# Optimization experiments

Measured on AMD Instinct MI355X. Metric: run time of the kernel, lower is better.

## Reference

```python
import math
import jax, jax.numpy as jnp
import numpy as np

B, N, D = 8, 2048, 256
NUM_ROLES = 3
ROLE_HUB, ROLE_MONITOR = 1, 2  # assumed ROLE_TO_ID mapping
NEG = -10000.0


def _lin_init(k, fan_in, shape):
    b = 1.0 / math.sqrt(fan_in)
    return jax.random.uniform(k, shape, jnp.float32, -b, b)


def setup_inputs() -> dict:
    key = jax.random.key(0)
    ks = jax.random.split(key, 20)
    inp = {
        'x': jax.random.normal(ks[0], (B, N, D), jnp.float32),
        'node_roles': jax.random.randint(ks[1], (B, N), 0, NUM_ROLES),
        'node_mask': jax.random.bernoulli(ks[2], 0.9, (B, N)),
        'ln_gamma': jnp.ones((D,), jnp.float32),
        'ln_beta': jnp.zeros((D,), jnp.float32),
        'role_emb': jax.random.normal(ks[3], (NUM_ROLES, D), jnp.float32),
    }
    names = ['q', 'k', 's', 'p', 'o']
    for i, nm in enumerate(names):
        inp['W' + nm] = _lin_init(ks[4 + 2 * i], D, (D, D))
        inp['b' + nm] = _lin_init(ks[5 + 2 * i], D, (D,))
    inp['Wg'] = _lin_init(ks[14], 2 * D, (2 * D, D))
    inp['bg'] = _lin_init(ks[15], 2 * D, (D,))
    return inp


def _layernorm(x, g, b):
    mu = jnp.mean(x, -1, keepdims=True)
    var = jnp.mean(jnp.square(x - mu), -1, keepdims=True)
    return (x - mu) * jax.lax.rsqrt(var + 1e-5) * g + b


def reference(x, node_roles, node_mask, ln_gamma, ln_beta, role_emb,
              Wq, bq, Wk, bk, Ws, bs, Wp, bp, Wo, bo, Wg, bg):
    normed = _layernorm(x, ln_gamma, ln_beta)
    role_bias = role_emb[node_roles]                      # [B,N,D]
    h = normed + role_bias
    query = h @ Wq + bq
    key_t = h @ Wk + bk
    sender = h @ Ws + bs
    payload = normed @ Wp + bp

    read_logits = jnp.einsum('bid,bjd->bij', query, key_t) / math.sqrt(D)
    fs = role_bias + sender
    forward_logits = jnp.einsum('bid,bjd->bij', fs, fs)
    logits = read_logits + 0.5 * forward_logits           # variant='selective'

    source_mask = node_mask                               # variant != 'memory_hubs'
    pair_mask = node_mask[:, :, None] & source_mask[:, None, :]
    eye = jnp.eye(N, dtype=bool)[None]
    pair_mask = pair_mask | (eye & node_mask[:, :, None] & node_mask[:, None, :])

    logits = jnp.where(pair_mask, logits, NEG)
    weights = jax.nn.softmax(logits, axis=-1)
    weights = jnp.where(pair_mask, weights, 0.0)

    message = jnp.einsum('bij,bjd->bid', weights, payload)
    gate = jax.nn.sigmoid(jnp.concatenate([x, message], axis=-1) @ Wg + bg)
    update = (gate * message) @ Wo + bo
    out = x + update                                      # dropout p=0

    entropy = -(weights * jnp.log(weights + 1e-8)).sum(-1).mean()
    # masked-mean replicates torch's weights[..., col_mask].mean() without dynamic shapes
    mon_cols = (node_roles == ROLE_MONITOR).any(0)        # [N]
    hub_cols = (node_roles == ROLE_HUB).any(0)
    def col_mean(cols):
        cnt = cols.sum() * B * N
        tot = (weights * cols[None, None, :].astype(weights.dtype)).sum()
        return jnp.where(cnt > 0, tot / jnp.maximum(cnt, 1), 0.0)
    return (out, entropy, col_mean(mon_cols), col_mean(hub_cols))
```

## Files before the change

### kernel.cpp

```cpp
#include <hip/hip_runtime.h>
#include <math.h>

#define BB 8
#define NN 2048
#define DD 256
#define MTOK 16384

typedef __bf16 bf16x8 __attribute__((ext_vector_type(8)));
typedef __bf16 bf16x4 __attribute__((ext_vector_type(4)));
typedef float f32x4 __attribute__((ext_vector_type(4)));

#define MFMA16(a, b, c) __builtin_amdgcn_mfma_f32_16x16x32_bf16(a, b, c, 0, 0, 0)

#define BARX()                              \
  do {                                      \
    asm volatile("" ::: "memory");          \
    __builtin_amdgcn_s_barrier();           \
    asm volatile("" ::: "memory");          \
  } while (0)
#define WAITVM(N)                                              \
  do {                                                         \
    asm volatile("s_waitcnt vmcnt(" #N ")" ::: "memory");      \
    __builtin_amdgcn_sched_barrier(0);                         \
  } while (0)

#define OFF_X16    0ull
#define OFF_N16    2097152ull
#define OFF_H16    4194304ull
#define OFF_GROW   8388608ull
#define OFF_GCOL   12582912ull
#define OFF_PTE    16777216ull
#define OFF_WT     19005440ull
#define OFF_STAT   19234816ull
#define OFF_ENT    23625728ull
#define OFF_MONR   23642112ull
#define OFF_HUBR   23658496ull
#define OFF_MONF   23674880ull
#define OFF_HUBF   23676928ull
#define OFF_MASK   23678976ull
#define OFF_PART   23683072ull
#define OFF_MSGN0  OFF_N16
#define OFF_MSGN1  OFF_H16
#define OFF_MSG16  OFF_PTE
#define OFF_GM16   OFF_GROW

__device__ __forceinline__ void gl_lds16(const void* g, void* l) {
  __builtin_amdgcn_global_load_lds(
      (const __attribute__((address_space(1))) unsigned int*)g,
      (__attribute__((address_space(3))) unsigned int*)l, 16, 0, 0);
}

__global__ __launch_bounds__(256) void setup_kernel(
    const float* __restrict__ x, const int* __restrict__ roles,
    const void* __restrict__ mraw,
    const float* __restrict__ gamma, const float* __restrict__ beta,
    const float* __restrict__ role_emb,
    const float* __restrict__ Wq, const float* __restrict__ Wk,
    const float* __restrict__ Ws, const float* __restrict__ Wp,
    const float* __restrict__ Wg, const float* __restrict__ Wo,
    __bf16* __restrict__ X16, __bf16* __restrict__ N16,
    __bf16* __restrict__ H16, __bf16* __restrict__ WT,
    unsigned char* __restrict__ mask8,
    float* __restrict__ monf, float* __restrict__ hubf) {
  __shared__ float T[64][65];
  int bid = blockIdx.x;
  int tid = threadIdx.x;
  if (bid < 4096) {
    int t = bid * 4 + (tid >> 6);
    int lane = tid & 63;
    size_t off = (size_t)t * DD + lane * 4;
    float4 xv = *(const float4*)(x + off);
    float s = xv.x + xv.y + xv.z + xv.w;
    float ss = xv.x * xv.x + xv.y * xv.y + xv.z * xv.z + xv.w * xv.w;
#pragma unroll
    for (int m = 1; m < 64; m <<= 1) {
      s += __shfl_xor(s, m, 64);
      ss += __shfl_xor(ss, m, 64);
    }
    float mu = s * (1.0f / 256.0f);
    float var = ss * (1.0f / 256.0f) - mu * mu;
    float inv = rsqrtf(var + 1e-5f);
    float4 g = *(const float4*)(gamma + lane * 4);
    float4 be = *(const float4*)(beta + lane * 4);
    float nv[4];
    nv[0] = (xv.x - mu) * inv * g.x + be.x;
    nv[1] = (xv.y - mu) * inv * g.y + be.y;
    nv[2] = (xv.z - mu) * inv * g.z + be.z;
    nv[3] = (xv.w - mu) * inv * g.w + be.w;
    int role = roles[t];
    float4 rb = *(const float4*)(role_emb + (size_t)role * DD + lane * 4);
    float rbv[4] = {rb.x, rb.y, rb.z, rb.w};
    bf16x4 xo, no, ho;
    float xf[4] = {xv.x, xv.y, xv.z, xv.w};
#pragma unroll
    for (int q = 0; q < 4; ++q) {
      xo[q] = (__bf16)xf[q];
      no[q] = (__bf16)nv[q];
      ho[q] = (__bf16)(nv[q] + rbv[q]);
    }
    *(bf16x4*)&X16[off] = xo;
    *(bf16x4*)&N16[off] = no;
    *(bf16x4*)&H16[off] = ho;
  } else if (bid < 4288) {
    int wblk = bid - 4096;
    int z = wblk >> 5, rem = wblk & 31;
    int bx = rem & 3, by = rem >> 2;
    const float* src;
    int K;
    size_t doff;
    switch (z) {
      case 0: src = Wq; K = 256; doff = 0; break;
      case 1: src = Wk; K = 256; doff = 65536; break;
      case 2: src = Ws; K = 256; doff = 131072; break;
      case 3: src = Wp; K = 256; doff = 196608; break;
      case 4: src = Wg; K = 512; doff = 262144; break;
      default: src = Wo; K = 256; doff = 393216; break;
    }
    int k0 = by * 64;
    if (k0 >= K) return;
    int n0 = bx * 64;
#pragma unroll
    for (int p = 0; p < 16; ++p) {
      int idx = p * 256 + tid;
      int r = idx >> 6, c = idx & 63;
      T[r][c] = src[(size_t)(k0 + r) * 256 + n0 + c];
    }
    __syncthreads();
#pragma unroll
    for (int p = 0; p < 16; ++p) {
      int idx = p * 256 + tid;
      int n = idx >> 6, k = idx & 63;
      WT[doff + (size_t)(n0 + n) * K + k0 + k] = (__bf16)T[k][n];
    }
  } else {
    int* csh = (int*)&T[0][0];
    if (tid == 0) { csh[0] = 0; csh[1] = 0; }
    __syncthreads();
    const unsigned char* raw = (const unsigned char*)mraw;
    int c0 = 0, c1 = 0;
    for (int i = tid; i < 4096; i += 256) {
      int nz = (raw[i] != 0) ? 1 : 0;
      if ((i & 3) == 0) c0 += nz; else c1 += nz;
    }
    atomicAdd(&csh[0], c0);
    atomicAdd(&csh[1], c1);
    __syncthreads();
    int k = (csh[0] == 0) ? 2 : ((csh[1] == 0) ? 0 : 1);
    int t = (bid - 4288) * 256 + tid;
    if (t < MTOK) {
      int v;
      if (k == 1)      v = (raw[t] != 0);
      else if (k == 0) v = (((const int*)mraw)[t] != 0);
      else             v = (((const float*)mraw)[t] != 0.0f);
      mask8[t] = (unsigned char)v;
    }
    if (t < NN) {
      int mon = 0, hub = 0;
#pragma unroll
      for (int b = 0; b < BB; ++b) {
        int r = roles[b * NN + t];
        mon |= (r == 2) ? 1 : 0;
        hub |= (r == 1) ? 1 : 0;
      }
      monf[t] = (float)mon;
      hubf[t] = (float)hub;
    }
  }
}

__global__ __launch_bounds__(256) void fill_pte_kernel(
    const int* __restrict__ roles, __bf16* __restrict__ PTE) {
  int idx = blockIdx.x * 256 + threadIdx.x;
  int b = idx >> 11, col = idx & 2047;
  int mon = 0, hub = 0;
#pragma unroll
  for (int bb = 0; bb < BB; ++bb) {
    int r = roles[bb * NN + col];
    mon |= (r == 2) ? 1 : 0;
    hub |= (r == 1) ? 1 : 0;
  }
  size_t rbase = ((size_t)(b * 272 + 256)) * 2048 + col;
  PTE[rbase] = (__bf16)(float)mon;
  PTE[rbase + 2048] = (__bf16)(float)hub;
  PTE[rbase + 2 * 2048] = (__bf16)1.0f;
#pragma unroll
  for (int r = 3; r < 16; ++r) PTE[rbase + (size_t)r * 2048] = (__bf16)0.0f;
}

__global__ __launch_bounds__(256, 3) void proj4_kernel(
    const __bf16* __restrict__ H16, const __bf16* __restrict__ N16,
    const __bf16* __restrict__ WT,
    const float* __restrict__ bq, const float* __restrict__ bk,
    const float* __restrict__ bs, const float* __restrict__ bp,
    const int* __restrict__ roles, const float* __restrict__ remb,
    __bf16* __restrict__ Grow, __bf16* __restrict__ Gcol,
    __bf16* __restrict__ PTE) {
  __shared__ __align__(16) unsigned char As[128 * 128];
  __shared__ __align__(16) unsigned char Bs[128 * 128];
  int z = blockIdx.z;
  const __bf16* A = (z == 3) ? N16 : H16;
  const __bf16* W = WT + (size_t)z * 65536;
  const float* bias = (z == 0) ? bq : (z == 1) ? bk : (z == 2) ? bs : bp;

  int tid = threadIdx.x;
  int w = tid >> 6, lane = tid & 63, ln15 = lane & 15, lq = lane >> 4;
  int wr = w >> 1, wc = w & 1;
  int row0 = blockIdx.y * 128, col0 = blockIdx.x * 128;
  f32x4 acc[4][4];
#pragma unroll
  for (int i = 0; i < 4; ++i)
#pragma unroll
    for (int j = 0; j < 4; ++j) acc[i][j] = (f32x4){0.f, 0.f, 0.f, 0.f};

  int lr = lane >> 3;
  int sb = ((lane & 7) * 16) ^ ((lr & 7) << 4);

  for (int kt = 0; kt < 4; ++kt) {
    __syncthreads();
#pragma unroll
    for (int i2 = 0; i2 < 4; ++i2) {
      int idx = w * 4 + i2;
      int grow = row0 + idx * 8 + lr;
      gl_lds16((const unsigned char*)A + (size_t)grow * 512 + kt * 128 + sb,
               As + idx * 1024);
    }
#pragma unroll
    for (int i2 = 0; i2 < 4; ++i2) {
      int idx = w * 4 + i2;
      int gcol = col0 + idx * 8 + lr;
      gl_lds16((const unsigned char*)W + (size_t)gcol * 512 + kt * 128 + sb,
               Bs + idx * 1024);
    }
    __syncthreads();
#pragma unroll
    for (int ks = 0; ks < 2; ++ks) {
      bf16x8 af[4], bfr[4];
#pragma unroll
      for (int i = 0; i < 4; ++i) {
        int rl = wr * 64 + i * 16 + ln15;
        int byteoff = (lq * 16 + ks * 64) ^ ((rl & 7) << 4);
        af[i] = *(const bf16x8*)(As + rl * 128 + byteoff);
      }
#pragma unroll
      for (int j = 0; j < 4; ++j) {
        int cl = wc * 64 + j * 16 + ln15;
        int byteoff = (lq * 16 + ks * 64) ^ ((cl & 7) << 4);
        bfr[j] = *(const bf16x8*)(Bs + cl * 128 + byteoff);
      }
#pragma unroll
      for (int i = 0; i < 4; ++i)
#pragma unroll
        for (int j = 0; j < 4; ++j) acc[i][j] = MFMA16(af[i], bfr[j], acc[i][j]);
    }
  }
  float bj[4];
#pragma unroll
  for (int j = 0; j < 4; ++j) bj[j] = bias[col0 + wc * 64 + j * 16 + ln15];
#pragma unroll
  for (int i = 0; i < 4; ++i) {
#pragma unroll
    for (int j = 0; j < 4; ++j) {
      int gcol = col0 + wc * 64 + j * 16 + ln15;
      int growb = row0 + wr * 64 + i * 16 + lq * 4;
      float o[4];
#pragma unroll
      for (int ri = 0; ri < 4; ++ri) o[ri] = acc[i][j][ri] + bj[j];
      if (z == 0) {
#pragma unroll
        for (int ri = 0; ri < 4; ++ri)
          Grow[(size_t)(growb + ri) * 512 + gcol] = (__bf16)(o[ri] * 0.0625f);
      } else if (z == 1) {
#pragma unroll
        for (int ri = 0; ri < 4; ++ri)
          Gcol[(size_t)(growb + ri) * 512 + gcol] = (__bf16)o[ri];
      } else if (z == 2) {
#pragma unroll
        for (int ri = 0; ri < 4; ++ri) {
          float oo = o[ri] + remb[(size_t)roles[growb + ri] * 256 + gcol];
          __bf16 v = (__bf16)(oo * 0.70710678118f);
          Grow[(size_t)(growb + ri) * 512 + 256 + gcol] = v;
          Gcol[(size_t)(growb + ri) * 512 + 256 + gcol] = v;
        }
      } else {
        bf16x4 v;
#pragma unroll
        for (int ri = 0; ri < 4; ++ri) v[ri] = (__bf16)o[ri];
        int b = growb >> 11, tok = growb & 2047;
        *(bf16x4*)&PTE[((size_t)(b * 272 + gcol)) * 2048 + tok] = v;
      }
    }
  }
}

__global__ __launch_bounds__(256, 2) void attn_kernel(
    const __bf16* __restrict__ Grow, const __bf16* __restrict__ Gcol,
    const __bf16* __restrict__ PTE, const unsigned char* __restrict__ mask8,
    __bf16* __restrict__ msgn0, __bf16* __restrict__ msgn1,
    float* __restrict__ statP) {
  __shared__ __align__(16) unsigned char GcLo[16384];
  __shared__ __align__(16) unsigned char GcHi[16384];
  __shared__ __align__(16) unsigned char PtS[2][17408];

  int tid = threadIdx.x;
  int w = tid >> 6, lane = tid & 63, ln15 = lane & 15, lq = lane >> 4;
  int id = blockIdx.x;
  int b = id & 7;
  int half = (id >> 3) & 1;
  int r0 = (id >> 4) * 64;
  size_t base = (size_t)b * NN;
  __bf16* msgn = half ? msgn1 : msgn0;
  float* statB = statP + (size_t)half * MTOK * 6;

  const unsigned char* gbase =
      (const unsigned char*)Gcol + (base + half * 1024) * 1024;
  const unsigned char* pbase =
      (const unsigned char*)PTE + (size_t)b * 272 * 4096 + half * 2048;

  bf16x8 Af[16];
  {
    const __bf16* gr = Grow + (base + r0 + w * 16 + ln15) * 512 + lq * 8;
#pragma unroll
    for (int kk = 0; kk < 16; ++kk) Af[kk] = *(const bf16x8*)(gr + kk * 32);
  }

  float m = -1e30f, T = 0.f;
  f32x4 macc[17];
#pragma unroll
  for (int nt = 0; nt < 17; ++nt) macc[nt] = (f32x4){0.f, 0.f, 0.f, 0.f};

  int pswz = (lq ^ ((ln15 >> 1) & 3)) << 4;
  int n0 = ((ln15 >> 2) * 8) + (ln15 & 3);
  int n1 = n0 + 4;
  int s0 = (((n0 & 3) | (((n0 >> 3) & 1) << 2))) << 4;
  int s1 = (((n1 & 3) | (((n1 >> 3) & 1) << 2))) << 4;
  int srcsw = ((lane & 3) ^ ((lane >> 3) & 3)) << 4;
  int glrow = lane >> 5;
  int glb = (lane & 31) * 16;

  auto STG = [&](int ch, unsigned char* dst, int koff) {
#pragma unroll
    for (int i = 0; i < 4; ++i) {
      int rp = w * 8 + 2 * i;
      int r = rp + glrow;
      int sbr = glb ^ ((((r & 3) | (((r >> 3) & 1) << 2))) << 4);
      gl_lds16(gbase + (size_t)(ch * 32 + r) * 1024 + koff + sbr, dst + rp * 512);
    }
  };
  auto STPT = [&](int ch, int buf) {
#pragma unroll
    for (int i = 0; i < 4; ++i) {
      int idx = w * 4 + i;
      int drow = idx * 16 + (lane >> 2);
      gl_lds16(pbase + (size_t)drow * 4096 + ch * 64 + srcsw,
               &PtS[buf][idx * 1024]);
    }
    {
      int drow = 256 + (lane >> 2);
      gl_lds16(pbase + (size_t)drow * 4096 + ch * 64 + srcsw,
               &PtS[buf][16 * 1024]);
    }
  };

  STPT(0, 0);
  STG(0, GcLo, 0);
  STG(0, GcHi, 512);

  for (int ch = 0; ch < 32; ++ch) {
    int cur = ch & 1;
    WAITVM(4);
    BARX();
    STPT(ch + 1, cur ^ 1);

    f32x4 sa0 = (f32x4){0.f, 0.f, 0.f, 0.f};
    f32x4 sa1 = (f32x4){0.f, 0.f, 0.f, 0.f};
    __builtin_amdgcn_s_setprio(1);
#pragma unroll
    for (int kk = 0; kk < 8; ++kk) {
      bf16x8 bv0 = *(const bf16x8*)&GcLo[n0 * 512 + ((lq * 16 + kk * 64) ^ s0)];
      sa0 = MFMA16(bv0, Af[kk], sa0);
      bf16x8 bv1 = *(const bf16x8*)&GcLo[n1 * 512 + ((lq * 16 + kk * 64) ^ s1)];
      sa1 = MFMA16(bv1, Af[kk], sa1);
    }
    __builtin_amdgcn_s_setprio(0);

    WAITVM(5);
    BARX();
    STG(ch + 1, GcLo, 0);

    __builtin_amdgcn_s_setprio(1);
#pragma unroll
    for (int kk = 8; kk < 16; ++kk) {
      bf16x8 bv0 = *(const bf16x8*)&GcHi[n0 * 512 + ((lq * 16 + (kk - 8) * 64) ^ s0)];
      sa0 = MFMA16(bv0, Af[kk], sa0);
      bf16x8 bv1 = *(const bf16x8*)&GcHi[n1 * 512 + ((lq * 16 + (kk - 8) * 64) ^ s1)];
      sa1 = MFMA16(bv1, Af[kk], sa1);
    }
    __builtin_amdgcn_s_setprio(0);

    float sv[8] = {sa0[0], sa0[1], sa0[2], sa0[3], sa1[0], sa1[1], sa1[2], sa1[3]};
    unsigned long long mk = *(const unsigned long long*)(
        mask8 + base + half * 1024 + (size_t)ch * 32 + lq * 8);

    float mt = -1e30f;
#pragma unroll
    for (int i = 0; i < 8; ++i) {
      float li = ((mk >> (8 * i)) & 0xffull) ? sv[i] : -1e30f;
      mt = fmaxf(mt, li);
    }
    mt = fmaxf(mt, __shfl_xor(mt, 16));
    mt = fmaxf(mt, __shfl_xor(mt, 32));
    float mnew = fmaxf(m, mt);
    if (__any(mnew > m + 8.0f)) {
      float ci = __expf(m - mnew);
      float cir[4];
#pragma unroll
      for (int r = 0; r < 4; ++r)
        cir[r] = __shfl(ci, (lane & 48) + ((lane >> 2) & 12) + r);
#pragma unroll
      for (int nt = 0; nt < 17; ++nt) {
        macc[nt][0] *= cir[0]; macc[nt][1] *= cir[1];
        macc[nt][2] *= cir[2]; macc[nt][3] *= cir[3];
      }
      T *= ci;
      m = mnew;
    }
    float e[8], tl = 0.f;
#pragma unroll
    for (int i = 0; i < 8; ++i) {
      float ei = ((mk >> (8 * i)) & 0xffull) ? __expf(sv[i] - m) : 0.f;
      e[i] = ei;
      tl += ei * sv[i];
    }
    tl += __shfl_xor(tl, 16);
    tl += __shfl_xor(tl, 32);
    T += tl;
    bf16x8 ef;
#pragma unroll
    for (int i = 0; i < 8; ++i) ef[i] = (__bf16)e[i];

    __builtin_amdgcn_s_setprio(1);
#pragma unroll
    for (int nt = 0; nt < 17; ++nt) {
      int drow = nt * 16 + ln15;
      bf16x8 pv = *(const bf16x8*)&PtS[cur][drow * 64 + pswz];
      macc[nt] = MFMA16(ef, pv, macc[nt]);
    }
    __builtin_amdgcn_s_setprio(0);

    BARX();
    STG(ch + 1, GcHi, 512);
  }
  WAITVM(0);

#pragma unroll
  for (int r = 0; r < 4; ++r) {
    int grow = r0 + w * 16 + lq * 4 + r;
    size_t row = base + grow;
    float Z = __shfl(macc[16][r], (lane & 48) + 2);
    float invZ = (Z > 0.f) ? (1.0f / Z) : 0.f;
#pragma unroll
    for (int nt = 0; nt < 16; ++nt)
      msgn[row * 256 + nt * 16 + ln15] = (__bf16)(macc[nt][r] * invZ);
    float Tm = __shfl(macc[16][r], (lane & 48) + 0);
    float Th = __shfl(macc[16][r], (lane & 48) + 1);
    float Tr = __shfl(T, (lane & 48) + ((lane >> 2) & 12) + r);
    float mr = __shfl(m, (lane & 48) + ((lane >> 2) & 12) + r);
    if (ln15 == 0) {
      float* stt = statB + row * 6;
      stt[0] = mr; stt[1] = Tr; stt[2] = Z; stt[3] = Tm; stt[4] = Th;
    }
  }
}

__global__ __launch_bounds__(256) void merge_kernel(
    const __bf16* __restrict__ msgn0, const __bf16* __restrict__ msgn1,
    const float* __restrict__ statP, const unsigned char* __restrict__ mask8,
    __bf16* __restrict__ MSG16, float* __restrict__ entr,
    float* __restrict__ monr, float* __restrict__ hubr) {
  int row = blockIdx.x * 4 + (threadIdx.x >> 6);
  int lane = threadIdx.x & 63;
  const float* s0 = statP + (size_t)row * 6;
  const float* s1 = statP + (size_t)(MTOK + row) * 6;
  float m0 = s0[0], T0 = s0[1], Z0 = s0[2], Tm0 = s0[3], Th0 = s0[4];
  float m1 = s1[0], T1 = s1[1], Z1 = s1[2], Tm1 = s1[3], Th1 = s1[4];
  int valid = mask8[row] != 0;
  float mm = fmaxf(m0, m1);
  float c0 = __expf(m0 - mm), c1 = __expf(m1 - mm);
  float w0 = c0 * Z0, w1 = c1 * Z1;
  float Z = w0 + w1;
  int ok = valid && (Z > 0.f);
  float invZ = ok ? (1.0f / Z) : 0.0f;
  float rw0 = w0 * invZ, rw1 = w1 * invZ;
  bf16x4 p0 = *(const bf16x4*)(msgn0 + (size_t)row * 256 + lane * 4);
  bf16x4 p1 = *(const bf16x4*)(msgn1 + (size_t)row * 256 + lane * 4);
  bf16x4 o;
#pragma unroll
  for (int q = 0; q < 4; ++q)
    o[q] = (__bf16)(rw0 * (float)p0[q] + rw1 * (float)p1[q]);
  *(bf16x4*)&MSG16[(size_t)row * 256 + lane * 4] = o;
  if (lane == 0) {
    float T = c0 * T0 + c1 * T1;
    float Tm = c0 * Tm0 + c1 * Tm1;
    float Th = c0 * Th0 + c1 * Th1;
    entr[row] = ok ? (__logf(Z) + mm - T * invZ) : 0.0f;
    monr[row] = ok ? (Tm * invZ) : 0.0f;
    hubr[row] = ok ? (Th * invZ) : 0.0f;
  }
}

template <int K, int MODE>
__global__ __launch_bounds__(256) void gemmb_kernel(
    const __bf16* __restrict__ A0, const __bf16* __restrict__ A1,
    const __bf16* __restrict__ WT, const float* __restrict__ bias,
    const float* __restrict__ xf, const __bf16* __restrict__ msg16,
    void* __restrict__ dst0) {
  __shared__ __align__(16) unsigned char As[128 * 128];
  __shared__ __align__(16) unsigned char Bs[64 * 128];
  int tid = threadIdx.x;
  int w = tid >> 6, lane = tid & 63, ln15 = lane & 15, lq = lane >> 4;
  int wr = w >> 1, wc = w & 1;
  int row0 = blockIdx.y * 128, col0 = blockIdx.x * 64;
  f32x4 acc[4][2];
#pragma unroll
  for (int i = 0; i < 4; ++i)
#pragma unroll
    for (int j = 0; j < 2; ++j) acc[i][j] = (f32x4){0.f, 0.f, 0.f, 0.f};

  int lr = lane >> 3;
  int sb = ((lane & 7) * 16) ^ ((lr & 7) << 4);

  for (int kt = 0; kt < K / 64; ++kt) {
    const __bf16* Ab = A0;
    int ktl = kt;
    if (K == 512 && kt >= 4) { Ab = A1; ktl = kt - 4; }
    __syncthreads();
#pragma unroll
    for (int i2 = 0; i2 < 4; ++i2) {
      int idx = w * 4 + i2;
      int grow = row0 + idx * 8 + lr;
      gl_lds16((const unsigned char*)Ab + (size_t)grow * 512 + ktl * 128 + sb,
               As + idx * 1024);
    }
#pragma unroll
    for (int i2 = 0; i2 < 2; ++i2) {
      int idx = w * 2 + i2;
      int gcol = col0 + idx * 8 + lr;
      gl_lds16((const unsigned char*)WT + (size_t)gcol * (K * 2) + kt * 128 + sb,
               Bs + idx * 1024);
    }
    __syncthreads();
#pragma unroll
    for (int ks = 0; ks < 2; ++ks) {
      bf16x8 af[4], bfr[2];
#pragma unroll
      for (int i = 0; i < 4; ++i) {
        int rl = wr * 64 + i * 16 + ln15;
        int byteoff = (lq * 16 + ks * 64) ^ ((rl & 7) << 4);
        af[i] = *(const bf16x8*)(As + rl * 128 + byteoff);
      }
#pragma unroll
      for (int j = 0; j < 2; ++j) {
        int cl = wc * 32 + j * 16 + ln15;
        int byteoff = (lq * 16 + ks * 64) ^ ((cl & 7) << 4);
        bfr[j] = *(const bf16x8*)(Bs + cl * 128 + byteoff);
      }
#pragma unroll
      for (int i = 0; i < 4; ++i)
#pragma unroll
        for (int j = 0; j < 2; ++j) acc[i][j] = MFMA16(af[i], bfr[j], acc[i][j]);
    }
  }
  float bj[2];
#pragma unroll
  for (int j = 0; j < 2; ++j) bj[j] = bias[col0 + wc * 32 + j * 16 + ln15];
#pragma unroll
  for (int i = 0; i < 4; ++i) {
#pragma unroll
    for (int ri = 0; ri < 4; ++ri) {
      int grow = row0 + wr * 64 + i * 16 + lq * 4 + ri;
#pragma unroll
      for (int j = 0; j < 2; ++j) {
        int gcol = col0 + wc * 32 + j * 16 + ln15;
        float o = acc[i][j][ri] + bj[j];
        if (MODE == 4) {
          float sg = 1.0f / (1.0f + __expf(-o));
          float mv = (float)msg16[(size_t)grow * 256 + gcol];
          ((__bf16*)dst0)[(size_t)grow * 256 + gcol] = (__bf16)(sg * mv);
        } else {
          ((float*)dst0)[(size_t)grow * 256 + gcol] =
              o + xf[(size_t)grow * 256 + gcol];
        }
      }
    }
  }
}

__device__ __forceinline__ float block_sum(float v, float* sh) {
  __syncthreads();
  sh[threadIdx.x] = v;
  __syncthreads();
  for (int s = 128; s > 0; s >>= 1) {
    if ((int)threadIdx.x < s) sh[threadIdx.x] += sh[threadIdx.x + s];
    __syncthreads();
  }
  return sh[0];
}

__global__ __launch_bounds__(256) void reduce1_kernel(
    const float* __restrict__ entr, const float* __restrict__ monr,
    const float* __restrict__ hubr, float* __restrict__ partial) {
  __shared__ float sh[256];
  int t = blockIdx.x * 256 + threadIdx.x;
  float es = entr[t], ms = monr[t], hs = hubr[t];
  float e = block_sum(es, sh);
  float mo = block_sum(ms, sh);
  float hu = block_sum(hs, sh);
  if (threadIdx.x == 0) {
    partial[blockIdx.x * 4 + 0] = e;
    partial[blockIdx.x * 4 + 1] = mo;
    partial[blockIdx.x * 4 + 2] = hu;
  }
}

__global__ __launch_bounds__(256) void reduce2_kernel(
    const float* __restrict__ partial, const float* __restrict__ monf,
    const float* __restrict__ hubf, float* __restrict__ out3) {
  __shared__ float sh[256];
  float es = 0.f, ms = 0.f, hs = 0.f, cmf = 0.f, chf = 0.f;
  if (threadIdx.x < 64) {
    es = partial[threadIdx.x * 4 + 0];
    ms = partial[threadIdx.x * 4 + 1];
    hs = partial[threadIdx.x * 4 + 2];
  }
  for (int j = threadIdx.x; j < NN; j += 256) { cmf += monf[j]; chf += hubf[j]; }
  float esum = block_sum(es, sh);
  float msum = block_sum(ms, sh);
  float hsum = block_sum(hs, sh);
  float cmsum = block_sum(cmf, sh);
  float chsum = block_sum(chf, sh);
  if (threadIdx.x == 0) {
    out3[0] = esum / 16384.0f;
    out3[1] = (cmsum > 0.f) ? (msum / (cmsum * 16384.0f)) : 0.0f;
    out3[2] = (chsum > 0.f) ? (hsum / (chsum * 16384.0f)) : 0.0f;
  }
}

extern "C" void kernel_launch(void* const* d_in, const int* in_sizes, int n_in,
                              void* d_out, int out_size, void* d_ws, size_t ws_size,
                              hipStream_t stream) {
  const float* x = (const float*)d_in[0];
  const int* roles = (const int*)d_in[1];
  const void* mraw = d_in[2];
  const float* gamma = (const float*)d_in[3];
  const float* beta = (const float*)d_in[4];
  const float* remb = (const float*)d_in[5];
  const float* Wq = (const float*)d_in[6];
  const float* bq = (const float*)d_in[7];
  const float* Wk = (const float*)d_in[8];
  const float* bk = (const float*)d_in[9];
  const float* Ws = (const float*)d_in[10];
  const float* bs = (const float*)d_in[11];
  const float* Wp = (const float*)d_in[12];
  const float* bp = (const float*)d_in[13];
  const float* Wo = (const float*)d_in[14];
  const float* bo = (const float*)d_in[15];
  const float* Wg = (const float*)d_in[16];
  const float* bg = (const float*)d_in[17];

  float* ws = (float*)d_ws;
  __bf16* X16 = (__bf16*)(ws + OFF_X16);
  __bf16* N16 = (__bf16*)(ws + OFF_N16);
  __bf16* H16 = (__bf16*)(ws + OFF_H16);
  __bf16* Grow = (__bf16*)(ws + OFF_GROW);
  __bf16* Gcol = (__bf16*)(ws + OFF_GCOL);
  __bf16* PTE = (__bf16*)(ws + OFF_PTE);
  __bf16* WT = (__bf16*)(ws + OFF_WT);
  float* statP = ws + OFF_STAT;
  __bf16* msgn0 = (__bf16*)(ws + OFF_MSGN0);
  __bf16* msgn1 = (__bf16*)(ws + OFF_MSGN1);
  float* partial = ws + OFF_PART;
  __bf16* MSG16 = (__bf16*)(ws + OFF_MSG16);
  __bf16* GM16 = (__bf16*)(ws + OFF_GM16);
  float* entr = ws + OFF_ENT;
  float* monr = ws + OFF_MONR;
  float* hubr = ws + OFF_HUBR;
  float* monfp = ws + OFF_MONF;
  float* hubfp = ws + OFF_HUBF;
  unsigned char* mask8 = (unsigned char*)(ws + OFF_MASK);
  float* out = (float*)d_out;

  __bf16* WTg = WT + 262144;
  __bf16* WTo = WT + 393216;

  setup_kernel<<<4352, 256, 0, stream>>>(x, roles, mraw, gamma, beta, remb,
                                         Wq, Wk, Ws, Wp, Wg, Wo,
                                         X16, N16, H16, WT, mask8, monfp, hubfp);
  fill_pte_kernel<<<64, 256, 0, stream>>>(roles, PTE);
  proj4_kernel<<<dim3(2, 128, 4), 256, 0, stream>>>(
      H16, N16, WT, bq, bk, bs, bp, roles, remb, Grow, Gcol, PTE);
  attn_kernel<<<512, 256, 0, stream>>>(Grow, Gcol, PTE, mask8, msgn0, msgn1,
                                       statP);
  merge_kernel<<<4096, 256, 0, stream>>>(msgn0, msgn1, statP, mask8, MSG16,
                                         entr, monr, hubr);
  dim3 gg(4, 128);
  gemmb_kernel<512, 4><<<gg, 256, 0, stream>>>(X16, MSG16, WTg, bg, nullptr,
                                               MSG16, GM16);
  gemmb_kernel<256, 5><<<gg, 256, 0, stream>>>(GM16, nullptr, WTo, bo, x,
                                               nullptr, out);
  reduce1_kernel<<<64, 256, 0, stream>>>(entr, monr, hubr, partial);
  reduce2_kernel<<<1, 256, 0, stream>>>(partial, monfp, hubfp, out + 4194304);
}
```

Measured before the change: 166.1 us.

## Split attention keys four ways and single-buffer payload tiles for higher occupancy

The attention kernel now splits the key dimension into quarters instead of halves, doubling the grid to 1024 blocks. The payload tile in LDS is split into two single-buffered halves refilled mid-iteration, so LDS use drops and launch bounds allow three blocks per CU. The merge kernel combines four partial softmax results, and the entropy and column-mean statistics move into reduce1. This adds more partial-output traffic and more barriers per chunk in exchange for higher occupancy and parallelism.

Measured after the change: 326.3 us. +96.4%, slower.

```diff
diff --git a/kernel.cpp b/kernel.cpp
--- a/kernel.cpp
+++ b/kernel.cpp
@@ -27,14 +27,13 @@
 #define OFF_X16    0ull
 #define OFF_N16    2097152ull
 #define OFF_H16    4194304ull
+#define OFF_MSGN2  6291456ull
 #define OFF_GROW   8388608ull
 #define OFF_GCOL   12582912ull
 #define OFF_PTE    16777216ull
 #define OFF_WT     19005440ull
 #define OFF_STAT   19234816ull
-#define OFF_ENT    23625728ull
-#define OFF_MONR   23642112ull
-#define OFF_HUBR   23658496ull
+#define OFF_MSGN3  19628032ull
 #define OFF_MONF   23674880ull
 #define OFF_HUBF   23676928ull
 #define OFF_MASK   23678976ull
@@ -292,29 +291,32 @@
   }
 }
 
-__global__ __launch_bounds__(256, 2) void attn_kernel(
+__global__ __launch_bounds__(256, 3) void attn_kernel(
     const __bf16* __restrict__ Grow, const __bf16* __restrict__ Gcol,
     const __bf16* __restrict__ PTE, const unsigned char* __restrict__ mask8,
     __bf16* __restrict__ msgn0, __bf16* __restrict__ msgn1,
+    __bf16* __restrict__ msgn2, __bf16* __restrict__ msgn3,
     float* __restrict__ statP) {
   __shared__ __align__(16) unsigned char GcLo[16384];
   __shared__ __align__(16) unsigned char GcHi[16384];
-  __shared__ __align__(16) unsigned char PtS[2][17408];
+  __shared__ __align__(16) unsigned char PtA[8192];
+  __shared__ __align__(16) unsigned char PtB[9216];
 
   int tid = threadIdx.x;
   int w = tid >> 6, lane = tid & 63, ln15 = lane & 15, lq = lane >> 4;
   int id = blockIdx.x;
   int b = id & 7;
-  int half = (id >> 3) & 1;
-  int r0 = (id >> 4) * 64;
+  int quarter = (id >> 3) & 3;
+  int r0 = (id >> 5) * 64;
   size_t base = (size_t)b * NN;
-  __bf16* msgn = half ? msgn1 : msgn0;
-  float* statB = statP + (size_t)half * MTOK * 6;
+  __bf16* msgn = (quarter == 0) ? msgn0 : (quarter == 1) ? msgn1
+                 : (quarter == 2) ? msgn2 : msgn3;
+  float* statB = statP + (size_t)quarter * MTOK * 6;
 
   const unsigned char* gbase =
-      (const unsigned char*)Gcol + (base + half * 1024) * 1024;
+      (const unsigned char*)Gcol + (base + quarter * 512) * 1024;
   const unsigned char* pbase =
-      (const unsigned char*)PTE + (size_t)b * 272 * 4096 + half * 2048;
+      (const unsigned char*)PTE + (size_t)b * 272 * 4096 + quarter * 1024;
 
   bf16x8 Af[16];
   {
@@ -346,30 +348,38 @@
       gl_lds16(gbase + (size_t)(ch * 32 + r) * 1024 + koff + sbr, dst + rp * 512);
     }
   };
-  auto STPT = [&](int ch, int buf) {
-#pragma unroll
-    for (int i = 0; i < 4; ++i) {
-      int idx = w * 4 + i;
+  auto STPTA = [&](int ch) {
+#pragma unroll
+    for (int i = 0; i < 2; ++i) {
+      int idx = w * 2 + i;
       int drow = idx * 16 + (lane >> 2);
       gl_lds16(pbase + (size_t)drow * 4096 + ch * 64 + srcsw,
-               &PtS[buf][idx * 1024]);
+               PtA + idx * 1024);
+    }
+  };
+  auto STPTB = [&](int ch) {
+#pragma unroll
+    for (int i = 0; i < 2; ++i) {
+      int idx = 8 + w * 2 + i;
+      int drow = idx * 16 + (lane >> 2);
+      gl_lds16(pbase + (size_t)drow * 4096 + ch * 64 + srcsw,
+               PtB + (idx - 8) * 1024);
     }
     {
       int drow = 256 + (lane >> 2);
       gl_lds16(pbase + (size_t)drow * 4096 + ch * 64 + srcsw,
-               &PtS[buf][16 * 1024]);
+               PtB + 8 * 1024);
     }
   };
 
-  STPT(0, 0);
   STG(0, GcLo, 0);
   STG(0, GcHi, 512);
-
-  for (int ch = 0; ch < 32; ++ch) {
-    int cur = ch & 1;
-    WAITVM(4);
+  STPTA(0);
+  STPTB(0);
+
+  for (int ch = 0; ch < 16; ++ch) {
+    WAITVM(9);
     BARX();
-    STPT(ch + 1, cur ^ 1);
 
     f32x4 sa0 = (f32x4){0.f, 0.f, 0.f, 0.f};
     f32x4 sa1 = (f32x4){0.f, 0.f, 0.f, 0.f};
@@ -399,7 +409,7 @@
 
     float sv[8] = {sa0[0], sa0[1], sa0[2], sa0[3], sa1[0], sa1[1], sa1[2], sa1[3]};
     unsigned long long mk = *(const unsigned long long*)(
-        mask8 + base + half * 1024 + (size_t)ch * 32 + lq * 8);
+        mask8 + base + quarter * 512 + (size_t)ch * 32 + lq * 8);
 
     float mt = -1e30f;
 #pragma unroll
@@ -438,17 +448,34 @@
 #pragma unroll
     for (int i = 0; i < 8; ++i) ef[i] = (__bf16)e[i];
 
-    __builtin_amdgcn_s_setprio(1);
-#pragma unroll
-    for (int nt = 0; nt < 17; ++nt) {
-      int drow = nt * 16 + ln15;
-      bf16x8 pv = *(const bf16x8*)&PtS[cur][drow * 64 + pswz];
-      macc[nt] = MFMA16(ef, pv, macc[nt]);
-    }
-    __builtin_amdgcn_s_setprio(0);
-
+    WAITVM(7);
     BARX();
     STG(ch + 1, GcHi, 512);
+
+    __builtin_amdgcn_s_setprio(1);
+#pragma unroll
+    for (int nt = 0; nt < 8; ++nt) {
+      int drow = nt * 16 + ln15;
+      bf16x8 pv = *(const bf16x8*)&PtA[drow * 64 + pswz];
+      macc[nt] = MFMA16(ef, pv, macc[nt]);
+    }
+    __builtin_amdgcn_s_setprio(0);
+
+    WAITVM(8);
+    BARX();
+    STPTA(ch + 1);
+
+    __builtin_amdgcn_s_setprio(1);
+#pragma unroll
+    for (int nt = 8; nt < 17; ++nt) {
+      int drow = (nt - 8) * 16 + ln15;
+      bf16x8 pv = *(const bf16x8*)&PtB[drow * 64 + pswz];
+      macc[nt] = MFMA16(ef, pv, macc[nt]);
+    }
+    __builtin_amdgcn_s_setprio(0);
+
+    BARX();
+    STPTB(ch + 1);
   }
   WAITVM(0);
 
@@ -474,38 +501,38 @@
 
 __global__ __launch_bounds__(256) void merge_kernel(
     const __bf16* __restrict__ msgn0, const __bf16* __restrict__ msgn1,
+    const __bf16* __restrict__ msgn2, const __bf16* __restrict__ msgn3,
     const float* __restrict__ statP, const unsigned char* __restrict__ mask8,
-    __bf16* __restrict__ MSG16, float* __restrict__ entr,
-    float* __restrict__ monr, float* __restrict__ hubr) {
+    __bf16* __restrict__ MSG16) {
   int row = blockIdx.x * 4 + (threadIdx.x >> 6);
   int lane = threadIdx.x & 63;
-  const float* s0 = statP + (size_t)row * 6;
-  const float* s1 = statP + (size_t)(MTOK + row) * 6;
-  float m0 = s0[0], T0 = s0[1], Z0 = s0[2], Tm0 = s0[3], Th0 = s0[4];
-  float m1 = s1[0], T1 = s1[1], Z1 = s1[2], Tm1 = s1[3], Th1 = s1[4];
-  int valid = mask8[row] != 0;
-  float mm = fmaxf(m0, m1);
-  float c0 = __expf(m0 - mm), c1 = __expf(m1 - mm);
-  float w0 = c0 * Z0, w1 = c1 * Z1;
-  float Z = w0 + w1;
-  int ok = valid && (Z > 0.f);
+  float mq[4], Zq[4];
+#pragma unroll
+  for (int q = 0; q < 4; ++q) {
+    const float* s = statP + (size_t)q * MTOK * 6 + (size_t)row * 6;
+    mq[q] = s[0];
+    Zq[q] = s[2];
+  }
+  float mm = fmaxf(fmaxf(mq[0], mq[1]), fmaxf(mq[2], mq[3]));
+  float wq[4], Z = 0.f;
+#pragma unroll
+  for (int q = 0; q < 4; ++q) {
+    wq[q] = __expf(mq[q] - mm) * Zq[q];
+    Z += wq[q];
+  }
+  int ok = (mask8[row] != 0) && (Z > 0.f);
   float invZ = ok ? (1.0f / Z) : 0.0f;
-  float rw0 = w0 * invZ, rw1 = w1 * invZ;
   bf16x4 p0 = *(const bf16x4*)(msgn0 + (size_t)row * 256 + lane * 4);
   bf16x4 p1 = *(const bf16x4*)(msgn1 + (size_t)row * 256 + lane * 4);
+  bf16x4 p2 = *(const bf16x4*)(msgn2 + (size_t)row * 256 + lane * 4);
+  bf16x4 p3 = *(const bf16x4*)(msgn3 + (size_t)row * 256 + lane * 4);
+  float r0 = wq[0] * invZ, r1 = wq[1] * invZ, r2 = wq[2] * invZ, r3 = wq[3] * invZ;
   bf16x4 o;
 #pragma unroll
   for (int q = 0; q < 4; ++q)
-    o[q] = (__bf16)(rw0 * (float)p0[q] + rw1 * (float)p1[q]);
+    o[q] = (__bf16)(r0 * (float)p0[q] + r1 * (float)p1[q] +
+                    r2 * (float)p2[q] + r3 * (float)p3[q]);
   *(bf16x4*)&MSG16[(size_t)row * 256 + lane * 4] = o;
-  if (lane == 0) {
-    float T = c0 * T0 + c1 * T1;
-    float Tm = c0 * Tm0 + c1 * Tm1;
-    float Th = c0 * Th0 + c1 * Th1;
-    entr[row] = ok ? (__logf(Z) + mm - T * invZ) : 0.0f;
-    monr[row] = ok ? (Tm * invZ) : 0.0f;
-    hubr[row] = ok ? (Th * invZ) : 0.0f;
-  }
 }
 
 template <int K, int MODE>
@@ -607,14 +634,31 @@
 }
 
 __global__ __launch_bounds__(256) void reduce1_kernel(
-    const float* __restrict__ entr, const float* __restrict__ monr,
-    const float* __restrict__ hubr, float* __restrict__ partial) {
+    const float* __restrict__ statP, const unsigned char* __restrict__ mask8,
+    float* __restrict__ partial) {
   __shared__ float sh[256];
-  int t = blockIdx.x * 256 + threadIdx.x;
-  float es = entr[t], ms = monr[t], hs = hubr[t];
-  float e = block_sum(es, sh);
-  float mo = block_sum(ms, sh);
-  float hu = block_sum(hs, sh);
+  int row = blockIdx.x * 256 + threadIdx.x;
+  float mq[4], Tq[4], Zq[4], Tmq[4], Thq[4];
+#pragma unroll
+  for (int q = 0; q < 4; ++q) {
+    const float* s = statP + (size_t)q * MTOK * 6 + (size_t)row * 6;
+    mq[q] = s[0]; Tq[q] = s[1]; Zq[q] = s[2]; Tmq[q] = s[3]; Thq[q] = s[4];
+  }
+  float mm = fmaxf(fmaxf(mq[0], mq[1]), fmaxf(mq[2], mq[3]));
+  float Z = 0.f, T = 0.f, Tm = 0.f, Th = 0.f;
+#pragma unroll
+  for (int q = 0; q < 4; ++q) {
+    float c = __expf(mq[q] - mm);
+    Z += c * Zq[q]; T += c * Tq[q]; Tm += c * Tmq[q]; Th += c * Thq[q];
+  }
+  int ok = (mask8[row] != 0) && (Z > 0.f);
+  float invZ = ok ? (1.0f / Z) : 0.0f;
+  float entr = ok ? (__logf(Z) + mm - T * invZ) : 0.0f;
+  float mon = ok ? (Tm * invZ) : 0.0f;
+  float hub = ok ? (Th * invZ) : 0.0f;
+  float e = block_sum(entr, sh);
+  float mo = block_sum(mon, sh);
+  float hu = block_sum(hub, sh);
   if (threadIdx.x == 0) {
     partial[blockIdx.x * 4 + 0] = e;
     partial[blockIdx.x * 4 + 1] = mo;
@@ -678,12 +722,11 @@
   float* statP = ws + OFF_STAT;
   __bf16* msgn0 = (__bf16*)(ws + OFF_MSGN0);
   __bf16* msgn1 = (__bf16*)(ws + OFF_MSGN1);
+  __bf16* msgn2 = (__bf16*)(ws + OFF_MSGN2);
+  __bf16* msgn3 = (__bf16*)(ws + OFF_MSGN3);
   float* partial = ws + OFF_PART;
   __bf16* MSG16 = (__bf16*)(ws + OFF_MSG16);
   __bf16* GM16 = (__bf16*)(ws + OFF_GM16);
-  float* entr = ws + OFF_ENT;
-  float* monr = ws + OFF_MONR;
-  float* hubr = ws + OFF_HUBR;
   float* monfp = ws + OFF_MONF;
   float* hubfp = ws + OFF_HUBF;
   unsigned char* mask8 = (unsigned char*)(ws + OFF_MASK);
@@ -698,15 +741,15 @@
   fill_pte_kernel<<<64, 256, 0, stream>>>(roles, PTE);
   proj4_kernel<<<dim3(2, 128, 4), 256, 0, stream>>>(
       H16, N16, WT, bq, bk, bs, bp, roles, remb, Grow, Gcol, PTE);
-  attn_kernel<<<512, 256, 0, stream>>>(Grow, Gcol, PTE, mask8, msgn0, msgn1,
-                                       statP);
-  merge_kernel<<<4096, 256, 0, stream>>>(msgn0, msgn1, statP, mask8, MSG16,
-                                         entr, monr, hubr);
+  attn_kernel<<<1024, 256, 0, stream>>>(Grow, Gcol, PTE, mask8,
+                                        msgn0, msgn1, msgn2, msgn3, statP);
+  merge_kernel<<<4096, 256, 0, stream>>>(msgn0, msgn1, msgn2, msgn3, statP,
+                                         mask8, MSG16);
   dim3 gg(4, 128);
   gemmb_kernel<512, 4><<<gg, 256, 0, stream>>>(X16, MSG16, WTg, bg, nullptr,
                                                MSG16, GM16);
   gemmb_kernel<256, 5><<<gg, 256, 0, stream>>>(GM16, nullptr, WTo, bo, x,
                                                nullptr, out);
-  reduce1_kernel<<<64, 256, 0, stream>>>(entr, monr, hubr, partial);
+  reduce1_kernel<<<64, 256, 0, stream>>>(statP, mask8, partial);
   reduce2_kernel<<<1, 256, 0, stream>>>(partial, monfp, hubfp, out + 4194304);
 }
```
